# Kernel optimization log

Hardware: AMD Instinct MI355X
Metric: run time of the kernel (lower is better)

## Reference

```python
import jax, jax.numpy as jnp
import numpy as np

IN_CH = 64
INTER = IN_CH // 2
B, H, W = 2, 80, 80


def setup_inputs() -> dict:
    key = jax.random.key(0)
    k = jax.random.split(key, 5)
    s = 1.0 / np.sqrt(IN_CH)
    return {
        "x": jax.random.normal(k[0], (B, IN_CH, H, W), dtype=jnp.float32),
        "g_w": jax.random.normal(k[1], (INTER, IN_CH), dtype=jnp.float32) * s,
        "theta_w": jax.random.normal(k[2], (INTER, IN_CH), dtype=jnp.float32) * s,
        "phi_w": jax.random.normal(k[3], (INTER, IN_CH), dtype=jnp.float32) * s,
        "w_w": jax.random.normal(k[4], (IN_CH, INTER), dtype=jnp.float32) * (1.0 / np.sqrt(INTER)),
    }


def reference(x, g_w, theta_w, phi_w, w_w):
    # Non-local block: 1x1 convs (bias=False) are channel matmuls over N=H*W positions.
    Bc, C, Hh, Ww = x.shape
    N = Hh * Ww
    xf = x.reshape(Bc, C, N)                            # [B, C, N]
    g = jnp.einsum('ic,bcn->bni', g_w, xf)              # [B, N, inter]
    theta = jnp.einsum('ic,bcn->bni', theta_w, xf)      # [B, N, inter]
    phi = jnp.einsum('ic,bcn->bin', phi_w, xf)          # [B, inter, N]
    affinity = jax.nn.softmax(jnp.einsum('bni,bim->bnm', theta, phi), axis=-1)  # [B, N, N]
    y = jnp.einsum('bnm,bmi->bni', affinity, g)         # [B, N, inter]
    y = jnp.einsum('ci,bni->bcn', w_w, y).reshape(Bc, C, Hh, Ww)
    return x + y
```

## Files before the change

kernel.cpp:

```cpp
#include <hip/hip_runtime.h>
#include <math.h>

#define BATCH 2
#define CH    64
#define INTER 32
#define NPOS  6400
#define LOG2E 1.44269504088896f
#define SPLIT 25
#define TPB   2

typedef _Float16 f16x8 __attribute__((ext_vector_type(8)));
typedef _Float16 f16x2 __attribute__((ext_vector_type(2)));
typedef _Float16 h4    __attribute__((ext_vector_type(4)));
typedef float    f32x4 __attribute__((ext_vector_type(4)));

static __device__ __forceinline__ f16x2 pkrtz(float a, float b) {
    return __builtin_bit_cast(f16x2, __builtin_amdgcn_cvt_pkrtz(a, b));
}

__global__ __launch_bounds__(256) void nlb_proj_kernel(
    const float* __restrict__ x,
    const float* __restrict__ g_w,
    const float* __restrict__ th_w,
    const float* __restrict__ ph_w,
    _Float16* __restrict__ Qh, _Float16* __restrict__ Kh,
    _Float16* __restrict__ Vt)
{
    const int b  = blockIdx.z;
    const int p  = blockIdx.y;
    const int n0 = blockIdx.x * 64;
    const int t  = threadIdx.x;
    const int w  = __builtin_amdgcn_readfirstlane(t) >> 6;
    const int lane = t & 63;

    const float* wsrc = (p == 0) ? th_w : (p == 1) ? ph_w : g_w;
    const float* xg = x + (size_t)b * CH * NPOS + n0 + lane;

    float xr[64];
    #pragma unroll
    for (int c = 0; c < 64; c++) xr[c] = xg[(size_t)c * NPOS];

    __shared__ float buf[32][65];

    float accs[8];
    #pragma unroll
    for (int rr = 0; rr < 8; rr++) {
        const int row = w * 8 + rr;
        const float* wr = wsrc + row * 64;
        float a0 = 0.f, a1 = 0.f, a2 = 0.f, a3 = 0.f;
        #pragma unroll
        for (int c = 0; c < 16; c++) {
            a0 += wr[c]      * xr[c];
            a1 += wr[c + 16] * xr[c + 16];
            a2 += wr[c + 32] * xr[c + 32];
            a3 += wr[c + 48] * xr[c + 48];
        }
        accs[rr] = (a0 + a1) + (a2 + a3);
    }

    if (p == 2) {
        const int n   = n0 + lane;
        const int kk  = n & 127;
        const int g   = kk >> 4, qd = (kk >> 2) & 3, rr2 = kk & 3;
        const int slot = (g >> 1) * 32 + qd * 8 + (g & 1) * 4 + rr2;
        const size_t col = (size_t)(n >> 7) * 128 + slot;
        #pragma unroll
        for (int rr = 0; rr < 8; rr++)
            Vt[((size_t)b * 32 + w * 8 + rr) * NPOS + col] = (_Float16)accs[rr];
        return;
    }

    #pragma unroll
    for (int rr = 0; rr < 8; rr++) buf[w * 8 + rr][lane] = accs[rr];
    __syncthreads();

    const float scale = (p == 0) ? LOG2E : 1.f;
    _Float16* dst = (p == 0) ? Qh : Kh;
    const int pos = t >> 2, ic = t & 3;
    f16x8 hv;
    #pragma unroll
    for (int j = 0; j < 8; j++)
        hv[j] = (_Float16)(buf[ic * 8 + j][pos] * scale);
    *(f16x8*)(dst + ((size_t)b * NPOS + n0 + pos) * 32 + ic * 8) = hv;
}

__global__ __launch_bounds__(256) void nlb_flash_kernel(
    const _Float16* __restrict__ Qh, const _Float16* __restrict__ Kh,
    const _Float16* __restrict__ Vt,
    _Float16* __restrict__ Opart, float2* __restrict__ ml)
{
    __shared__ __align__(16) _Float16 ks[128][40];
    __shared__ __align__(16) _Float16 vs[32][136];

    const int b     = blockIdx.z;
    const int split = blockIdx.y;
    const int t     = threadIdx.x;
    const int w     = t >> 6;
    const int lane  = t & 63;
    const int n16   = lane & 15;
    const int quad  = lane >> 4;
    const int q0    = blockIdx.x * 64 + w * 16;

    const f16x8 qa = *(const f16x8*)(Qh + ((size_t)b * NPOS + q0 + n16) * 32 + quad * 8);

    const _Float16* KB = Kh + (size_t)b * NPOS * 32;
    const _Float16* VB = Vt + (size_t)b * 32 * NPOS;

    f32x4 o0 = (f32x4)0.f;
    f32x4 o1 = (f32x4)0.f;
    float runm = -1e30f, lsum = 0.f;

    const int key0 = t >> 2, part = t & 3, key1 = key0 + 64;
    const int dim0 = t >> 4, kp   = t & 15, dim1 = dim0 + 16;

    const int kt0 = split * TPB;
    f16x8 kr0, kr1, vr0, vr1;
    {
        const int k0 = kt0 * 128;
        kr0 = *(const f16x8*)(KB + (size_t)(k0 + key0) * 32 + part * 8);
        kr1 = *(const f16x8*)(KB + (size_t)(k0 + key1) * 32 + part * 8);
        vr0 = *(const f16x8*)(VB + (size_t)dim0 * NPOS + k0 + kp * 8);
        vr1 = *(const f16x8*)(VB + (size_t)dim1 * NPOS + k0 + kp * 8);
    }

    for (int i = 0; i < TPB; i++) {
        if (i) __syncthreads();
        *(f16x8*)&ks[key0][part * 8] = kr0;
        *(f16x8*)&ks[key1][part * 8] = kr1;
        *(f16x8*)&vs[dim0][kp * 8]   = vr0;
        *(f16x8*)&vs[dim1][kp * 8]   = vr1;
        __syncthreads();

        if (i + 1 < TPB) {
            const int k0n = (kt0 + i + 1) * 128;
            kr0 = *(const f16x8*)(KB + (size_t)(k0n + key0) * 32 + part * 8);
            kr1 = *(const f16x8*)(KB + (size_t)(k0n + key1) * 32 + part * 8);
            vr0 = *(const f16x8*)(VB + (size_t)dim0 * NPOS + k0n + kp * 8);
            vr1 = *(const f16x8*)(VB + (size_t)dim1 * NPOS + k0n + kp * 8);
        }

        f32x4 sc[8];
        #pragma unroll
        for (int g = 0; g < 8; g++) {
            f16x8 kf = *(const f16x8*)&ks[g * 16 + n16][quad * 8];
            f32x4 z = (f32x4)0.f;
            sc[g] = __builtin_amdgcn_mfma_f32_16x16x32_f16(kf, qa, z, 0, 0, 0);
        }

        float m = fmaxf(fmaxf(sc[0][0], sc[0][1]), fmaxf(sc[0][2], sc[0][3]));
        #pragma unroll
        for (int g = 1; g < 8; g++) {
            float mg = fmaxf(fmaxf(sc[g][0], sc[g][1]), fmaxf(sc[g][2], sc[g][3]));
            m = fmaxf(m, mg);
        }
        m = fmaxf(m, __shfl_xor(m, 16));
        m = fmaxf(m, __shfl_xor(m, 32));
        float nm = fmaxf(runm, m);
        float a  = __builtin_amdgcn_exp2f(runm - nm);
        runm = nm;
        float ls = 0.f;
        #pragma unroll
        for (int g = 0; g < 8; g++) {
            #pragma unroll
            for (int r = 0; r < 4; r++) {
                float p = __builtin_amdgcn_exp2f(sc[g][r] - nm);
                sc[g][r] = p;
                ls += p;
            }
        }
        lsum = lsum * a + ls;
        o0 *= a;
        o1 *= a;

        #pragma unroll
        for (int kc = 0; kc < 4; kc++) {
            union { f16x8 v; f16x2 h2[4]; } pb;
            pb.h2[0] = pkrtz(sc[kc * 2][0],     sc[kc * 2][1]);
            pb.h2[1] = pkrtz(sc[kc * 2][2],     sc[kc * 2][3]);
            pb.h2[2] = pkrtz(sc[kc * 2 + 1][0], sc[kc * 2 + 1][1]);
            pb.h2[3] = pkrtz(sc[kc * 2 + 1][2], sc[kc * 2 + 1][3]);
            f16x8 v0 = *(const f16x8*)&vs[n16][kc * 32 + quad * 8];
            f16x8 v1 = *(const f16x8*)&vs[16 + n16][kc * 32 + quad * 8];
            o0 = __builtin_amdgcn_mfma_f32_16x16x32_f16(v0, pb.v, o0, 0, 0, 0);
            o1 = __builtin_amdgcn_mfma_f32_16x16x32_f16(v1, pb.v, o1, 0, 0, 0);
        }
    }

    lsum += __shfl_xor(lsum, 16);
    lsum += __shfl_xor(lsum, 32);
    float invl = 1.f / lsum;
    const size_t base = ((size_t)(b * SPLIT + split) * NPOS + q0 + n16) * 32;
    h4 h0, h1;
    #pragma unroll
    for (int r = 0; r < 4; r++) {
        h0[r] = (_Float16)(o0[r] * invl);
        h1[r] = (_Float16)(o1[r] * invl);
    }
    *(h4*)(Opart + base + quad * 4)      = h0;
    *(h4*)(Opart + base + 16 + quad * 4) = h1;
    if (quad == 0)
        ml[(size_t)(b * SPLIT + split) * NPOS + q0 + n16] = make_float2(runm, lsum);
}

__global__ __launch_bounds__(256) void nlb_combine_kernel(
    const _Float16* __restrict__ Opart, const float2* __restrict__ ml,
    const float* __restrict__ w_w, const float* __restrict__ x,
    float* __restrict__ out)
{
    __shared__ float wf[64][33];
    __shared__ float wts[32][SPLIT + 2];
    __shared__ float of[32][33];

    const int b  = blockIdx.y;
    const int q0 = blockIdx.x * 32;
    const int t  = threadIdx.x;

    for (int idx = t; idx < 2048; idx += 256) wf[idx >> 5][idx & 31] = w_w[idx];

    if (t < 32) {
        float2 v[SPLIT];
        float m = -1e30f;
        #pragma unroll
        for (int s = 0; s < SPLIT; s++) {
            v[s] = ml[(size_t)(b * SPLIT + s) * NPOS + q0 + t];
            m = fmaxf(m, v[s].x);
        }
        float suml = 0.f;
        #pragma unroll
        for (int s = 0; s < SPLIT; s++) {
            float wgt = __builtin_amdgcn_exp2f(v[s].x - m) * v[s].y;
            wts[t][s] = wgt;
            suml += wgt;
        }
        float inv = 1.f / suml;
        #pragma unroll
        for (int s = 0; s < SPLIT; s++) wts[t][s] *= inv;
    }
    __syncthreads();

    {
        const int q = t >> 3, dg = t & 7;
        float a0 = 0.f, a1 = 0.f, a2 = 0.f, a3 = 0.f;
        #pragma unroll
        for (int s = 0; s < SPLIT; s++) {
            h4 hv = *(const h4*)(Opart +
                ((size_t)(b * SPLIT + s) * NPOS + q0 + q) * 32 + dg * 4);
            float c = wts[q][s];
            a0 += c * (float)hv[0]; a1 += c * (float)hv[1];
            a2 += c * (float)hv[2]; a3 += c * (float)hv[3];
        }
        of[q][dg * 4]     = a0; of[q][dg * 4 + 1] = a1;
        of[q][dg * 4 + 2] = a2; of[q][dg * 4 + 3] = a3;
    }
    __syncthreads();

    {
        const int q = t & 31, cg = t >> 5;
        const float* xb = x   + (size_t)b * CH * NPOS + q0 + q;
        float*       ob = out + (size_t)b * CH * NPOS + q0 + q;
        #pragma unroll
        for (int cc = 0; cc < 8; cc++) {
            int ch = cg * 8 + cc;
            float acc = 0.f;
            #pragma unroll
            for (int i = 0; i < 32; i++) acc += wf[ch][i] * of[q][i];
            ob[(size_t)ch * NPOS] = acc + xb[(size_t)ch * NPOS];
        }
    }
}

extern "C" void kernel_launch(void* const* d_in, const int* in_sizes, int n_in,
                              void* d_out, int out_size, void* d_ws, size_t ws_size,
                              hipStream_t stream) {
    const float* x    = (const float*)d_in[0];
    const float* g_w  = (const float*)d_in[1];
    const float* th_w = (const float*)d_in[2];
    const float* ph_w = (const float*)d_in[3];
    const float* w_w  = (const float*)d_in[4];
    float* out = (float*)d_out;

    const size_t SZ = (size_t)BATCH * NPOS * INTER;
    _Float16* Qh = (_Float16*)d_ws;
    _Float16* Kh = Qh + SZ;
    _Float16* Vt = Kh + SZ;
    _Float16* Opart = Vt + SZ;
    float2*   ml    = (float2*)(Opart + SZ * SPLIT);

    nlb_proj_kernel<<<dim3(NPOS / 64, 3, BATCH), 256, 0, stream>>>(
        x, g_w, th_w, ph_w, Qh, Kh, Vt);
    nlb_flash_kernel<<<dim3(NPOS / 64, SPLIT, BATCH), 256, 0, stream>>>(
        Qh, Kh, Vt, Opart, ml);
    nlb_combine_kernel<<<dim3(NPOS / 32, BATCH), 256, 0, stream>>>(
        Opart, ml, w_w, x, out);
}
```

Before: 114.4 us.

## Split keys across waves within block and merge partial softmax in LDS

The flash kernel now has each wave process all 64 queries of the block against its own slice of key chunks, loading K and V fragments straight from global memory into registers instead of staging shared tiles. The four waves' partial outputs and max/sum statistics are merged in shared memory before writing, which cuts the number of global splits from 25 to 10. This removes the per-tile LDS staging and barriers and shrinks the partial buffers the combine kernel must read. In exchange it adds an in-block reduction and uses more registers per wave, and the global K/V loads are less coalesced.

```diff
diff --git a/kernel.cpp b/kernel.cpp
--- a/kernel.cpp
+++ b/kernel.cpp
@@ -6,8 +6,8 @@
 #define INTER 32
 #define NPOS  6400
 #define LOG2E 1.44269504088896f
-#define SPLIT 25
-#define TPB   2
+#define SPLIT 10
+#define CPW   5
 
 typedef _Float16 f16x8 __attribute__((ext_vector_type(8)));
 typedef _Float16 f16x2 __attribute__((ext_vector_type(2)));
@@ -89,8 +89,8 @@
     const _Float16* __restrict__ Vt,
     _Float16* __restrict__ Opart, float2* __restrict__ ml)
 {
-    __shared__ __align__(16) _Float16 ks[128][40];
-    __shared__ __align__(16) _Float16 vs[32][136];
+    __shared__ __align__(16) float Om[4][64][36];
+    __shared__ float Ml[4][64][2];
 
     const int b     = blockIdx.z;
     const int split = blockIdx.y;
@@ -99,107 +99,125 @@
     const int lane  = t & 63;
     const int n16   = lane & 15;
     const int quad  = lane >> 4;
-    const int q0    = blockIdx.x * 64 + w * 16;
-
-    const f16x8 qa = *(const f16x8*)(Qh + ((size_t)b * NPOS + q0 + n16) * 32 + quad * 8);
+    const int q0    = blockIdx.x * 64;
+
+    f16x8 qa[4];
+    #pragma unroll
+    for (int qg = 0; qg < 4; qg++)
+        qa[qg] = *(const f16x8*)(Qh + ((size_t)b * NPOS + q0 + qg * 16 + n16) * 32 + quad * 8);
 
     const _Float16* KB = Kh + (size_t)b * NPOS * 32;
     const _Float16* VB = Vt + (size_t)b * 32 * NPOS;
 
-    f32x4 o0 = (f32x4)0.f;
-    f32x4 o1 = (f32x4)0.f;
-    float runm = -1e30f, lsum = 0.f;
-
-    const int key0 = t >> 2, part = t & 3, key1 = key0 + 64;
-    const int dim0 = t >> 4, kp   = t & 15, dim1 = dim0 + 16;
-
-    const int kt0 = split * TPB;
-    f16x8 kr0, kr1, vr0, vr1;
+    f32x4 o[4][2];
+    #pragma unroll
+    for (int qg = 0; qg < 4; qg++) { o[qg][0] = (f32x4)0.f; o[qg][1] = (f32x4)0.f; }
+    float runm[4] = {-1e30f, -1e30f, -1e30f, -1e30f};
+    float lsum[4] = {0.f, 0.f, 0.f, 0.f};
+
+    const int c0 = split * 20 + w * CPW;
+
+    f16x8 ka0, ka1, va0, va1;
     {
-        const int k0 = kt0 * 128;
-        kr0 = *(const f16x8*)(KB + (size_t)(k0 + key0) * 32 + part * 8);
-        kr1 = *(const f16x8*)(KB + (size_t)(k0 + key1) * 32 + part * 8);
-        vr0 = *(const f16x8*)(VB + (size_t)dim0 * NPOS + k0 + kp * 8);
-        vr1 = *(const f16x8*)(VB + (size_t)dim1 * NPOS + k0 + kp * 8);
-    }
-
-    for (int i = 0; i < TPB; i++) {
-        if (i) __syncthreads();
-        *(f16x8*)&ks[key0][part * 8] = kr0;
-        *(f16x8*)&ks[key1][part * 8] = kr1;
-        *(f16x8*)&vs[dim0][kp * 8]   = vr0;
-        *(f16x8*)&vs[dim1][kp * 8]   = vr1;
-        __syncthreads();
-
-        if (i + 1 < TPB) {
-            const int k0n = (kt0 + i + 1) * 128;
-            kr0 = *(const f16x8*)(KB + (size_t)(k0n + key0) * 32 + part * 8);
-            kr1 = *(const f16x8*)(KB + (size_t)(k0n + key1) * 32 + part * 8);
-            vr0 = *(const f16x8*)(VB + (size_t)dim0 * NPOS + k0n + kp * 8);
-            vr1 = *(const f16x8*)(VB + (size_t)dim1 * NPOS + k0n + kp * 8);
-        }
-
-        f32x4 sc[8];
-        #pragma unroll
-        for (int g = 0; g < 8; g++) {
-            f16x8 kf = *(const f16x8*)&ks[g * 16 + n16][quad * 8];
+        ka0 = *(const f16x8*)(KB + (size_t)(c0 * 32 + n16) * 32 + quad * 8);
+        ka1 = *(const f16x8*)(KB + (size_t)(c0 * 32 + 16 + n16) * 32 + quad * 8);
+        va0 = *(const f16x8*)(VB + (size_t)n16 * NPOS + c0 * 32 + quad * 8);
+        va1 = *(const f16x8*)(VB + (size_t)(16 + n16) * NPOS + c0 * 32 + quad * 8);
+    }
+
+    for (int i = 0; i < CPW; i++) {
+        const int cn = c0 + i + 1;
+
+        f32x4 sc0[4], sc1[4];
+        #pragma unroll
+        for (int qg = 0; qg < 4; qg++) {
             f32x4 z = (f32x4)0.f;
-            sc[g] = __builtin_amdgcn_mfma_f32_16x16x32_f16(kf, qa, z, 0, 0, 0);
-        }
-
-        float m = fmaxf(fmaxf(sc[0][0], sc[0][1]), fmaxf(sc[0][2], sc[0][3]));
-        #pragma unroll
-        for (int g = 1; g < 8; g++) {
-            float mg = fmaxf(fmaxf(sc[g][0], sc[g][1]), fmaxf(sc[g][2], sc[g][3]));
-            m = fmaxf(m, mg);
-        }
-        m = fmaxf(m, __shfl_xor(m, 16));
-        m = fmaxf(m, __shfl_xor(m, 32));
-        float nm = fmaxf(runm, m);
-        float a  = __builtin_amdgcn_exp2f(runm - nm);
-        runm = nm;
-        float ls = 0.f;
-        #pragma unroll
-        for (int g = 0; g < 8; g++) {
+            sc0[qg] = __builtin_amdgcn_mfma_f32_16x16x32_f16(ka0, qa[qg], z, 0, 0, 0);
+            sc1[qg] = __builtin_amdgcn_mfma_f32_16x16x32_f16(ka1, qa[qg], z, 0, 0, 0);
+        }
+        if (i + 1 < CPW) {
+            ka0 = *(const f16x8*)(KB + (size_t)(cn * 32 + n16) * 32 + quad * 8);
+            ka1 = *(const f16x8*)(KB + (size_t)(cn * 32 + 16 + n16) * 32 + quad * 8);
+        }
+
+        #pragma unroll
+        for (int qg = 0; qg < 4; qg++) {
+            float m = fmaxf(fmaxf(sc0[qg][0], sc0[qg][1]), fmaxf(sc0[qg][2], sc0[qg][3]));
+            m = fmaxf(m, fmaxf(fmaxf(sc1[qg][0], sc1[qg][1]), fmaxf(sc1[qg][2], sc1[qg][3])));
+            m = fmaxf(m, __shfl_xor(m, 16));
+            m = fmaxf(m, __shfl_xor(m, 32));
+            float nm = fmaxf(runm[qg], m);
+            float a  = __builtin_amdgcn_exp2f(runm[qg] - nm);
+            runm[qg] = nm;
+            float ls = 0.f;
             #pragma unroll
             for (int r = 0; r < 4; r++) {
-                float p = __builtin_amdgcn_exp2f(sc[g][r] - nm);
-                sc[g][r] = p;
-                ls += p;
+                float p0 = __builtin_amdgcn_exp2f(sc0[qg][r] - nm);
+                float p1 = __builtin_amdgcn_exp2f(sc1[qg][r] - nm);
+                sc0[qg][r] = p0; sc1[qg][r] = p1;
+                ls += p0 + p1;
             }
-        }
-        lsum = lsum * a + ls;
-        o0 *= a;
-        o1 *= a;
-
-        #pragma unroll
-        for (int kc = 0; kc < 4; kc++) {
+            lsum[qg] = lsum[qg] * a + ls;
+            o[qg][0] *= a;
+            o[qg][1] *= a;
+
             union { f16x8 v; f16x2 h2[4]; } pb;
-            pb.h2[0] = pkrtz(sc[kc * 2][0],     sc[kc * 2][1]);
-            pb.h2[1] = pkrtz(sc[kc * 2][2],     sc[kc * 2][3]);
-            pb.h2[2] = pkrtz(sc[kc * 2 + 1][0], sc[kc * 2 + 1][1]);
-            pb.h2[3] = pkrtz(sc[kc * 2 + 1][2], sc[kc * 2 + 1][3]);
-            f16x8 v0 = *(const f16x8*)&vs[n16][kc * 32 + quad * 8];
-            f16x8 v1 = *(const f16x8*)&vs[16 + n16][kc * 32 + quad * 8];
-            o0 = __builtin_amdgcn_mfma_f32_16x16x32_f16(v0, pb.v, o0, 0, 0, 0);
-            o1 = __builtin_amdgcn_mfma_f32_16x16x32_f16(v1, pb.v, o1, 0, 0, 0);
-        }
-    }
-
-    lsum += __shfl_xor(lsum, 16);
-    lsum += __shfl_xor(lsum, 32);
-    float invl = 1.f / lsum;
-    const size_t base = ((size_t)(b * SPLIT + split) * NPOS + q0 + n16) * 32;
-    h4 h0, h1;
-    #pragma unroll
-    for (int r = 0; r < 4; r++) {
-        h0[r] = (_Float16)(o0[r] * invl);
-        h1[r] = (_Float16)(o1[r] * invl);
-    }
-    *(h4*)(Opart + base + quad * 4)      = h0;
-    *(h4*)(Opart + base + 16 + quad * 4) = h1;
-    if (quad == 0)
-        ml[(size_t)(b * SPLIT + split) * NPOS + q0 + n16] = make_float2(runm, lsum);
+            pb.h2[0] = pkrtz(sc0[qg][0], sc0[qg][1]);
+            pb.h2[1] = pkrtz(sc0[qg][2], sc0[qg][3]);
+            pb.h2[2] = pkrtz(sc1[qg][0], sc1[qg][1]);
+            pb.h2[3] = pkrtz(sc1[qg][2], sc1[qg][3]);
+            o[qg][0] = __builtin_amdgcn_mfma_f32_16x16x32_f16(va0, pb.v, o[qg][0], 0, 0, 0);
+            o[qg][1] = __builtin_amdgcn_mfma_f32_16x16x32_f16(va1, pb.v, o[qg][1], 0, 0, 0);
+        }
+        if (i + 1 < CPW) {
+            va0 = *(const f16x8*)(VB + (size_t)n16 * NPOS + cn * 32 + quad * 8);
+            va1 = *(const f16x8*)(VB + (size_t)(16 + n16) * NPOS + cn * 32 + quad * 8);
+        }
+    }
+
+    #pragma unroll
+    for (int qg = 0; qg < 4; qg++) {
+        float l = lsum[qg];
+        l += __shfl_xor(l, 16);
+        l += __shfl_xor(l, 32);
+        const int q = qg * 16 + n16;
+        if (quad == 0) { Ml[w][q][0] = runm[qg]; Ml[w][q][1] = l; }
+        *(float4*)&Om[w][q][quad * 4]      = *(float4*)&o[qg][0];
+        *(float4*)&Om[w][q][16 + quad * 4] = *(float4*)&o[qg][1];
+    }
+    __syncthreads();
+
+    {
+        const int q = t >> 2, dg = t & 3;
+        float m0 = Ml[0][q][0], m1 = Ml[1][q][0], m2 = Ml[2][q][0], m3 = Ml[3][q][0];
+        float ms = fmaxf(fmaxf(m0, m1), fmaxf(m2, m3));
+        float cw[4];
+        cw[0] = __builtin_amdgcn_exp2f(m0 - ms);
+        cw[1] = __builtin_amdgcn_exp2f(m1 - ms);
+        cw[2] = __builtin_amdgcn_exp2f(m2 - ms);
+        cw[3] = __builtin_amdgcn_exp2f(m3 - ms);
+        float l = cw[0] * Ml[0][q][1] + cw[1] * Ml[1][q][1]
+                + cw[2] * Ml[2][q][1] + cw[3] * Ml[3][q][1];
+        float acc[8];
+        #pragma unroll
+        for (int d = 0; d < 8; d++) acc[d] = 0.f;
+        #pragma unroll
+        for (int ww = 0; ww < 4; ww++) {
+            float c = cw[ww];
+            #pragma unroll
+            for (int d = 0; d < 8; d++) acc[d] += c * Om[ww][q][dg * 8 + d];
+        }
+        float invl = 1.f / l;
+        union { f16x8 v; f16x2 h2[4]; } ov;
+        ov.h2[0] = pkrtz(acc[0] * invl, acc[1] * invl);
+        ov.h2[1] = pkrtz(acc[2] * invl, acc[3] * invl);
+        ov.h2[2] = pkrtz(acc[4] * invl, acc[5] * invl);
+        ov.h2[3] = pkrtz(acc[6] * invl, acc[7] * invl);
+        const size_t base = ((size_t)(b * SPLIT + split) * NPOS + q0 + q) * 32;
+        *(f16x8*)(Opart + base + dg * 8) = ov.v;
+        if (dg == 0)
+            ml[(size_t)(b * SPLIT + split) * NPOS + q0 + q] = make_float2(ms, l);
+    }
 }
 
 __global__ __launch_bounds__(256) void nlb_combine_kernel(
```

After: 113.8 us. No clear change (-0.5%).
